# Optimization experiments

Measured on AMD Instinct MI355X. Metric: run time of the kernel, lower is better.

Reference implementation:

```python
import jax, jax.numpy as jnp
import numpy as np

B, C, T_IN = 32, 512, 1024
T_OUT = 4096  # fixed total expanded length (all rows of durations sum to this)


def setup_inputs() -> dict:
    key = jax.random.key(0)
    k_enc, k_cut = jax.random.split(key)
    encodings = jax.random.normal(k_enc, (B, C, T_IN), dtype=jnp.float32)
    # durations: nonnegative ints summing exactly to T_OUT per row, mean ~4.
    # Build as diffs of sorted random cut points in [0, T_OUT].
    cuts = jnp.sort(jax.random.randint(k_cut, (B, T_IN - 1), 0, T_OUT), axis=1)
    lo = jnp.zeros((B, 1), dtype=cuts.dtype)
    hi = jnp.full((B, 1), T_OUT, dtype=cuts.dtype)
    bounds = jnp.concatenate([lo, cuts, hi], axis=1)  # [B, T_IN+1]
    durations = (bounds[:, 1:] - bounds[:, :-1]).astype(jnp.int64)  # [B, T_IN]
    return {"encodings": encodings, "durations": durations}


def reference(encodings, durations):
    # Fused length regulation: instead of per-batch repeat_interleave + stack,
    # compute the gather index map from cumulative durations in one pass.
    # out[b, :, t] = encodings[b, :, j] where j = searchsorted(cumsum(dur[b]), t, 'right')
    cum = jnp.cumsum(durations, axis=1)  # [B, T_IN], last col == T_OUT
    t = jnp.arange(T_OUT)  # [T_OUT]
    idx = jax.vmap(lambda c: jnp.searchsorted(c, t, side="right"))(cum)  # [B, T_OUT]
    # gather along time axis, broadcast over channels
    return jnp.take_along_axis(encodings, idx[:, None, :], axis=2)  # [B, C, T_OUT]
```

## Files before the change

kernel.cpp:

```cpp
#include <hip/hip_runtime.h>

#define B_DIM 32
#define C_DIM 512
#define T_IN 1024
#define T_OUT 4096
#define CPB 4
#define PARTS 8

typedef float nfloat4 __attribute__((ext_vector_type(4)));
typedef int nint4 __attribute__((ext_vector_type(4)));

#define GLDS(lptr, gptr)                                                      \
    __builtin_amdgcn_global_load_lds(                                         \
        (const __attribute__((address_space(1))) unsigned int*)(gptr),        \
        (__attribute__((address_space(3))) unsigned int*)(lptr), 16, 0, 0)

__global__ __launch_bounds__(256) void build_idx_kernel(
    const int* __restrict__ dur, int* __restrict__ idx) {
    __shared__ __align__(16) int s_cum[T_IN];
    __shared__ int s_part[256];

    const int b = blockIdx.x;
    const int part = blockIdx.y;
    const int tid = threadIdx.x;

    nint4 v = ((const nint4*)(dur + b * T_IN))[tid];
    int c1 = v.x, c2 = c1 + v.y, c3 = c2 + v.z, c4 = c3 + v.w;

    s_part[tid] = c4;
    __syncthreads();
    #pragma unroll
    for (int off = 1; off < 256; off <<= 1) {
        int val = s_part[tid];
        int add = (tid >= off) ? s_part[tid - off] : 0;
        __syncthreads();
        s_part[tid] = val + add;
        __syncthreads();
    }
    int prefix = s_part[tid] - c4;

    nint4 cumv;
    cumv.x = prefix + c1;
    cumv.y = prefix + c2;
    cumv.z = prefix + c3;
    cumv.w = prefix + c4;
    ((nint4*)s_cum)[tid] = cumv;
    __syncthreads();

    int* row = idx + b * T_OUT + part * (T_OUT / PARTS);
    #pragma unroll
    for (int k = 0; k < T_OUT / PARTS / 256; ++k) {
        const int t = part * (T_OUT / PARTS) + k * 256 + tid;
        int lo = 0, hi = T_IN - 1;
        #pragma unroll
        for (int s = 0; s < 10; ++s) {
            int mid = (lo + hi) >> 1;
            bool gt = s_cum[mid] > t;
            hi = gt ? mid : hi;
            lo = gt ? lo : mid + 1;
        }
        row[k * 256 + tid] = lo;
    }
}

__global__ __launch_bounds__(256) void gather_kernel(
    const float* __restrict__ enc, const int* __restrict__ idx,
    float* __restrict__ out) {
    __shared__ __align__(16) float s_rows[CPB][T_IN];

    const int blk = blockIdx.x;
    const int b = blk >> 7;
    const int c0 = (blk & 127) * CPB;
    const int tid = threadIdx.x;
    const int wbase = (tid >> 6) << 8;

    const float* enc_base = enc + ((size_t)(b * C_DIM + c0)) * T_IN;

    GLDS(&s_rows[0][wbase], enc_base + 0 * T_IN + tid * 4);
    GLDS(&s_rows[1][wbase], enc_base + 1 * T_IN + tid * 4);

    const nint4* idx_row = (const nint4*)(idx + b * T_OUT);
    nint4 jj[4];
    #pragma unroll
    for (int g = 0; g < 4; ++g) jj[g] = idx_row[g * 256 + tid];

    __syncthreads();

    GLDS(&s_rows[2][wbase], enc_base + 2 * T_IN + tid * 4);
    GLDS(&s_rows[3][wbase], enc_base + 3 * T_IN + tid * 4);
    asm volatile("" ::: "memory");

    float* out_base = out + ((size_t)(b * C_DIM + c0)) * T_OUT;

    #pragma unroll
    for (int cc = 0; cc < 2; ++cc) {
        #pragma unroll
        for (int g = 0; g < 4; ++g) {
            nint4 j = jj[g];
            nfloat4 o;
            o.x = s_rows[cc][j.x];
            o.y = s_rows[cc][j.y];
            o.z = s_rows[cc][j.z];
            o.w = s_rows[cc][j.w];
            __builtin_nontemporal_store(
                o, ((nfloat4*)(out_base + (size_t)cc * T_OUT)) + g * 256 + tid);
        }
    }

    asm volatile("s_waitcnt vmcnt(8)" ::: "memory");
    __builtin_amdgcn_s_barrier();

    #pragma unroll
    for (int cc = 2; cc < CPB; ++cc) {
        #pragma unroll
        for (int g = 0; g < 4; ++g) {
            nint4 j = jj[g];
            nfloat4 o;
            o.x = s_rows[cc][j.x];
            o.y = s_rows[cc][j.y];
            o.z = s_rows[cc][j.z];
            o.w = s_rows[cc][j.w];
            __builtin_nontemporal_store(
                o, ((nfloat4*)(out_base + (size_t)cc * T_OUT)) + g * 256 + tid);
        }
    }
}

extern "C" void kernel_launch(void* const* d_in, const int* in_sizes, int n_in,
                              void* d_out, int out_size, void* d_ws, size_t ws_size,
                              hipStream_t stream) {
    const float* enc = (const float*)d_in[0];
    const int* dur = (const int*)d_in[1];
    float* out = (float*)d_out;
    int* idx = (int*)d_ws;

    build_idx_kernel<<<dim3(B_DIM, PARTS), 256, 0, stream>>>(dur, idx);
    gather_kernel<<<B_DIM * (C_DIM / CPB), 256, 0, stream>>>(enc, idx, out);
}
```

Before: 316.8 us.

## Fuse index building into gather kernel, recomputing cumsum per block

Merges the separate index-building kernel into the gather kernel, so each block reloads the durations row, runs its own prefix scan and binary search, and derives the gather indices in registers. This removes one kernel launch, the workspace round trip and the dependency between two launches. The price is that the scan and search are repeated in every one of the 4096 blocks, and the binary search is replaced by one search per four outputs followed by a linear walk. All four encoder rows are loaded asynchronously up front so the loads overlap the scan, and syncthreads is replaced with LDS-only waits during the scan.

```diff
diff --git a/kernel.cpp b/kernel.cpp
--- a/kernel.cpp
+++ b/kernel.cpp
@@ -5,7 +5,6 @@
 #define T_IN 1024
 #define T_OUT 4096
 #define CPB 4
-#define PARTS 8
 
 typedef float nfloat4 __attribute__((ext_vector_type(4)));
 typedef int nint4 __attribute__((ext_vector_type(4)));
@@ -15,27 +14,42 @@
         (const __attribute__((address_space(1))) unsigned int*)(gptr),        \
         (__attribute__((address_space(3))) unsigned int*)(lptr), 16, 0, 0)
 
-__global__ __launch_bounds__(256) void build_idx_kernel(
-    const int* __restrict__ dur, int* __restrict__ idx) {
+static __device__ __forceinline__ void lds_barrier() {
+    asm volatile("s_waitcnt lgkmcnt(0)" ::: "memory");
+    __builtin_amdgcn_s_barrier();
+}
+
+__global__ __launch_bounds__(256) void fused_regulate_kernel(
+    const float* __restrict__ enc, const int* __restrict__ dur,
+    float* __restrict__ out) {
+    __shared__ __align__(16) float s_rows[CPB][T_IN];
     __shared__ __align__(16) int s_cum[T_IN];
     __shared__ int s_part[256];
 
-    const int b = blockIdx.x;
-    const int part = blockIdx.y;
+    const int blk = blockIdx.x;
+    const int b = blk >> 7;
+    const int c0 = (blk & 127) * CPB;
     const int tid = threadIdx.x;
+    const int wbase = (tid >> 6) << 8;
 
     nint4 v = ((const nint4*)(dur + b * T_IN))[tid];
+
+    const float* enc_base = enc + ((size_t)(b * C_DIM + c0)) * T_IN;
+    GLDS(&s_rows[0][wbase], enc_base + 0 * T_IN + tid * 4);
+    GLDS(&s_rows[1][wbase], enc_base + 1 * T_IN + tid * 4);
+    GLDS(&s_rows[2][wbase], enc_base + 2 * T_IN + tid * 4);
+    GLDS(&s_rows[3][wbase], enc_base + 3 * T_IN + tid * 4);
+
     int c1 = v.x, c2 = c1 + v.y, c3 = c2 + v.z, c4 = c3 + v.w;
-
     s_part[tid] = c4;
-    __syncthreads();
+    lds_barrier();
     #pragma unroll
     for (int off = 1; off < 256; off <<= 1) {
         int val = s_part[tid];
         int add = (tid >= off) ? s_part[tid - off] : 0;
-        __syncthreads();
+        lds_barrier();
         s_part[tid] = val + add;
-        __syncthreads();
+        lds_barrier();
     }
     int prefix = s_part[tid] - c4;
 
@@ -45,81 +59,42 @@
     cumv.z = prefix + c3;
     cumv.w = prefix + c4;
     ((nint4*)s_cum)[tid] = cumv;
-    __syncthreads();
+    lds_barrier();
 
-    int* row = idx + b * T_OUT + part * (T_OUT / PARTS);
+    int j[4][4];
     #pragma unroll
-    for (int k = 0; k < T_OUT / PARTS / 256; ++k) {
-        const int t = part * (T_OUT / PARTS) + k * 256 + tid;
+    for (int g = 0; g < 4; ++g) {
+        const int t0 = (g * 256 + tid) * 4;
         int lo = 0, hi = T_IN - 1;
         #pragma unroll
         for (int s = 0; s < 10; ++s) {
             int mid = (lo + hi) >> 1;
-            bool gt = s_cum[mid] > t;
+            bool gt = s_cum[mid] > t0;
             hi = gt ? mid : hi;
             lo = gt ? lo : mid + 1;
         }
-        row[k * 256 + tid] = lo;
+        int jj = lo;
+        j[g][0] = jj;
+        #pragma unroll
+        for (int q = 1; q < 4; ++q) {
+            const int t = t0 + q;
+            while (s_cum[jj] <= t) ++jj;
+            j[g][q] = jj;
+        }
     }
-}
-
-__global__ __launch_bounds__(256) void gather_kernel(
-    const float* __restrict__ enc, const int* __restrict__ idx,
-    float* __restrict__ out) {
-    __shared__ __align__(16) float s_rows[CPB][T_IN];
-
-    const int blk = blockIdx.x;
-    const int b = blk >> 7;
-    const int c0 = (blk & 127) * CPB;
-    const int tid = threadIdx.x;
-    const int wbase = (tid >> 6) << 8;
-
-    const float* enc_base = enc + ((size_t)(b * C_DIM + c0)) * T_IN;
-
-    GLDS(&s_rows[0][wbase], enc_base + 0 * T_IN + tid * 4);
-    GLDS(&s_rows[1][wbase], enc_base + 1 * T_IN + tid * 4);
-
-    const nint4* idx_row = (const nint4*)(idx + b * T_OUT);
-    nint4 jj[4];
-    #pragma unroll
-    for (int g = 0; g < 4; ++g) jj[g] = idx_row[g * 256 + tid];
 
     __syncthreads();
 
-    GLDS(&s_rows[2][wbase], enc_base + 2 * T_IN + tid * 4);
-    GLDS(&s_rows[3][wbase], enc_base + 3 * T_IN + tid * 4);
-    asm volatile("" ::: "memory");
-
     float* out_base = out + ((size_t)(b * C_DIM + c0)) * T_OUT;
-
     #pragma unroll
-    for (int cc = 0; cc < 2; ++cc) {
+    for (int cc = 0; cc < CPB; ++cc) {
         #pragma unroll
         for (int g = 0; g < 4; ++g) {
-            nint4 j = jj[g];
             nfloat4 o;
-            o.x = s_rows[cc][j.x];
-            o.y = s_rows[cc][j.y];
-            o.z = s_rows[cc][j.z];
-            o.w = s_rows[cc][j.w];
-            __builtin_nontemporal_store(
-                o, ((nfloat4*)(out_base + (size_t)cc * T_OUT)) + g * 256 + tid);
-        }
-    }
-
-    asm volatile("s_waitcnt vmcnt(8)" ::: "memory");
-    __builtin_amdgcn_s_barrier();
-
-    #pragma unroll
-    for (int cc = 2; cc < CPB; ++cc) {
-        #pragma unroll
-        for (int g = 0; g < 4; ++g) {
-            nint4 j = jj[g];
-            nfloat4 o;
-            o.x = s_rows[cc][j.x];
-            o.y = s_rows[cc][j.y];
-            o.z = s_rows[cc][j.z];
-            o.w = s_rows[cc][j.w];
+            o.x = s_rows[cc][j[g][0]];
+            o.y = s_rows[cc][j[g][1]];
+            o.z = s_rows[cc][j[g][2]];
+            o.w = s_rows[cc][j[g][3]];
             __builtin_nontemporal_store(
                 o, ((nfloat4*)(out_base + (size_t)cc * T_OUT)) + g * 256 + tid);
         }
@@ -132,8 +107,7 @@
     const float* enc = (const float*)d_in[0];
     const int* dur = (const int*)d_in[1];
     float* out = (float*)d_out;
-    int* idx = (int*)d_ws;
+    (void)d_ws; (void)ws_size;
 
-    build_idx_kernel<<<dim3(B_DIM, PARTS), 256, 0, stream>>>(dur, idx);
-    gather_kernel<<<B_DIM * (C_DIM / CPB), 256, 0, stream>>>(enc, idx, out);
+    fused_regulate_kernel<<<B_DIM * (C_DIM / CPB), 256, 0, stream>>>(enc, dur, out);
 }
```

Result: no change. 316.4 us (-0.1%).
